# Performance work log

Measured on AMD Instinct MI355X. Metric: run time of the kernel, lower is better.

The kernel has to match this reference:

```python
import jax, jax.numpy as jnp
import numpy as np

NUM_HEADS = 16
ROPE_THETA = 10000.0


def _rope_angles(seq_len, head_dim, dtype):
    # lucidrains rotary_embedding_torch: freqs = theta^(-2i/d) for i in 0..d/2,
    # angles = pos * freq, then each angle repeated twice along last dim (interleaved pairs).
    inv_freq = 1.0 / (ROPE_THETA ** (jnp.arange(0, head_dim, 2, dtype=jnp.float32) / head_dim))
    angles = jnp.arange(seq_len, dtype=jnp.float32)[:, None] * inv_freq  # [N, D/2]
    return jnp.repeat(angles, 2, axis=-1).astype(dtype)  # [N, D]


def _rotate_half(t):
    # interleaved pairs: (x0, x1) -> (-x1, x0)
    t1 = t[..., ::2]
    t2 = t[..., 1::2]
    return jnp.stack([-t2, t1], axis=-1).reshape(t.shape)


def _apply_rope(t, cos, sin):
    # t: [B, H, N, D]; cos/sin: [N, D]
    return t * cos + _rotate_half(t) * sin


def setup_inputs() -> dict:
    key = jax.random.key(0)
    ks = jax.random.split(key, 5)
    B, N, C = 4, 1024, 1024
    return {
        "x": jax.random.normal(ks[0], (B, N, C), dtype=jnp.float32),
        "w_qkv": jax.random.normal(ks[1], (C, 3 * C), dtype=jnp.float32) * (C ** -0.5),
        "b_qkv": jax.random.normal(ks[2], (3 * C,), dtype=jnp.float32) * 0.02,
        "w_proj": jax.random.normal(ks[3], (C, C), dtype=jnp.float32) * (C ** -0.5),
        "b_proj": jax.random.normal(ks[4], (C,), dtype=jnp.float32) * 0.02,
    }


def reference(x, w_qkv, b_qkv, w_proj, b_proj):
    B, N, C = x.shape
    H = NUM_HEADS
    D = C // H

    qkv = x @ w_qkv + b_qkv  # [B, N, 3C]
    qkv = qkv.reshape(B, N, 3, H, D).transpose(2, 0, 3, 1, 4)  # [3, B, H, N, D]
    q, k, v = qkv[0], qkv[1], qkv[2]

    ang = _rope_angles(N, D, x.dtype)
    cos, sin = jnp.cos(ang), jnp.sin(ang)
    q = _apply_rope(q, cos, sin)
    k = _apply_rope(k, cos, sin)

    scale = D ** -0.5  # SDPA default scale
    scores = jnp.einsum("bhqd,bhkd->bhqk", q, k) * scale
    attn = jax.nn.softmax(scores, axis=-1)
    out = jnp.einsum("bhqk,bhkd->bhqd", attn, v)  # [B, H, N, D]

    out = out.transpose(0, 2, 1, 3).reshape(B, N, C)
    return out @ w_proj + b_proj
```

## Files before the change

kernel.cpp:

```cpp
#include <hip/hip_runtime.h>
#include <math.h>

#define BB 4
#define NN 1024
#define CC 1024
#define HH 16
#define DD 64
#define N3 3072

typedef __attribute__((ext_vector_type(8))) short bf16x8;
typedef __attribute__((ext_vector_type(8))) _Float16 f16x8;
typedef __attribute__((ext_vector_type(4))) _Float16 f16x4;
typedef __attribute__((ext_vector_type(4))) float f32x4;
typedef __attribute__((ext_vector_type(4))) unsigned int u32x4;

struct ushort4_t { unsigned short x, y, z, w; };

static __device__ __forceinline__ unsigned short f2b(float f) {
    union { float f; unsigned int u; } v; v.f = f;
    unsigned int r = (v.u + 0x7fffu + ((v.u >> 16) & 1u)) >> 16;
    return (unsigned short)r;
}

static __device__ __forceinline__ void ldg_lds16(const void* g, void* l) {
    __builtin_amdgcn_global_load_lds(
        (const __attribute__((address_space(1))) unsigned int*)g,
        (__attribute__((address_space(3))) unsigned int*)l, 16, 0, 0);
}

__global__ __launch_bounds__(256) void prep(const float* __restrict__ x,
                                            const float* __restrict__ wq,
                                            const float* __restrict__ wp,
                                            _Float16* __restrict__ Xh,
                                            _Float16* __restrict__ Wqt,
                                            _Float16* __restrict__ Wpt,
                                            float* __restrict__ ct,
                                            float* __restrict__ st) {
    const int blk = blockIdx.x;
    const int t = threadIdx.x;
    if (blk < 4096) {
        int tid = blk * 256 + t;
        float4 v = ((const float4*)x)[tid];
        f16x4 o = {(_Float16)v.x, (_Float16)v.y, (_Float16)v.z, (_Float16)v.w};
        ((f16x4*)Xh)[tid] = o;
    } else if (blk < 5632) {
        int idx = blk - 4096;
        int n  = (idx % 12) * 256 + t;
        int k0 = (idx / 12) * 8;
        f16x8 o;
        #pragma unroll
        for (int kk = 0; kk < 8; kk++)
            o[kk] = (_Float16)wq[(size_t)(k0 + kk) * N3 + n];
        *(f16x8*)(Wqt + (size_t)n * 1024 + k0) = o;
    } else if (blk < 6144) {
        int idx = blk - 5632;
        int n  = (idx % 4) * 256 + t;
        int k0 = (idx / 4) * 8;
        f16x8 o;
        #pragma unroll
        for (int kk = 0; kk < 8; kk++)
            o[kk] = (_Float16)wp[(size_t)(k0 + kk) * 1024 + n];
        *(f16x8*)(Wpt + (size_t)n * 1024 + k0) = o;
    } else {
        int tid = (blk - 6144) * 256 + t;
        int n = tid >> 5, i = tid & 31;
        double ang = (double)n * exp2(-(double)i * (13.287712379549449 / 32.0));
        ct[tid] = (float)cos(ang);
        st[tid] = (float)sin(ang);
    }
}

static __device__ __forceinline__ void gemm_body_pipe(const char* gA, const char* gB,
                                                      int m0, int n0,
                                                      _Float16* As0, _Float16* As1,
                                                      _Float16* Bs0, _Float16* Bs1,
                                                      int tid, int ln, int qd,
                                                      int wm, int wn, f32x4 acc[4][4]) {
    const int lrow   = tid >> 3;
    const int lchunk = tid & 7;
    const int swz    = (lchunk ^ (lrow & 7)) * 8;

    u32x4 pa[4], pb[4];

    #pragma unroll
    for (int c = 0; c < 4; c++) {
        size_t ra = (size_t)(m0 + c * 32 + lrow) * 2048 + lchunk * 16;
        size_t rb = (size_t)(n0 + c * 32 + lrow) * 2048 + lchunk * 16;
        pa[c] = *(const u32x4*)(gA + ra);
        pb[c] = *(const u32x4*)(gB + rb);
    }
    #pragma unroll
    for (int c = 0; c < 4; c++) {
        *(u32x4*)&As0[(c * 32 + lrow) * 64 + swz] = pa[c];
        *(u32x4*)&Bs0[(c * 32 + lrow) * 64 + swz] = pb[c];
    }
    #pragma unroll
    for (int c = 0; c < 4; c++) {
        size_t ra = (size_t)(m0 + c * 32 + lrow) * 2048 + 128 + lchunk * 16;
        size_t rb = (size_t)(n0 + c * 32 + lrow) * 2048 + 128 + lchunk * 16;
        pa[c] = *(const u32x4*)(gA + ra);
        pb[c] = *(const u32x4*)(gB + rb);
    }
    __syncthreads();

    #pragma unroll
    for (int t = 0; t < 16; t++) {
        const _Float16* Ac = (t & 1) ? As1 : As0;
        const _Float16* Bc = (t & 1) ? Bs1 : Bs0;

        #pragma unroll
        for (int kc = 0; kc < 2; kc++) {
            f16x8 af[4], bf[4];
            #pragma unroll
            for (int i = 0; i < 4; i++)
                af[i] = *(const f16x8*)&Ac[(wm + i * 16 + ln) * 64 +
                                           (((kc * 4 + qd) ^ (ln & 7)) * 8)];
            #pragma unroll
            for (int j = 0; j < 4; j++)
                bf[j] = *(const f16x8*)&Bc[(wn + j * 16 + ln) * 64 +
                                           (((kc * 4 + qd) ^ (ln & 7)) * 8)];
            #pragma unroll
            for (int i = 0; i < 4; i++)
                #pragma unroll
                for (int j = 0; j < 4; j++)
                    acc[i][j] = __builtin_amdgcn_mfma_f32_16x16x32_f16(af[i], bf[j],
                                                                       acc[i][j], 0, 0, 0);
        }

        if (t < 15) {
            _Float16* An = (t & 1) ? As0 : As1;
            _Float16* Bn = (t & 1) ? Bs0 : Bs1;
            #pragma unroll
            for (int c = 0; c < 4; c++) {
                *(u32x4*)&An[(c * 32 + lrow) * 64 + swz] = pa[c];
                *(u32x4*)&Bn[(c * 32 + lrow) * 64 + swz] = pb[c];
            }
            if (t < 14) {
                size_t ko = (size_t)(t + 2) * 128;
                #pragma unroll
                for (int c = 0; c < 4; c++) {
                    size_t ra = (size_t)(m0 + c * 32 + lrow) * 2048 + ko + lchunk * 16;
                    size_t rb = (size_t)(n0 + c * 32 + lrow) * 2048 + ko + lchunk * 16;
                    pa[c] = *(const u32x4*)(gA + ra);
                    pb[c] = *(const u32x4*)(gB + rb);
                }
            }
        }
        __syncthreads();
    }
}

static __device__ __forceinline__ void gemm_body_pipe_n64(const char* gA, const char* gB,
                                                          int m0, int n0,
                                                          _Float16* As0, _Float16* As1,
                                                          _Float16* Bs0, _Float16* Bs1,
                                                          int tid, int ln, int qd,
                                                          int wm, int wn, f32x4 acc[4][2]) {
    const int lrow   = tid >> 3;
    const int lchunk = tid & 7;
    const int swz    = (lchunk ^ (lrow & 7)) * 8;

    u32x4 pa[4], pb[2];

    #pragma unroll
    for (int c = 0; c < 4; c++)
        pa[c] = *(const u32x4*)(gA + (size_t)(m0 + c * 32 + lrow) * 2048 + lchunk * 16);
    #pragma unroll
    for (int c = 0; c < 2; c++)
        pb[c] = *(const u32x4*)(gB + (size_t)(n0 + c * 32 + lrow) * 2048 + lchunk * 16);
    #pragma unroll
    for (int c = 0; c < 4; c++)
        *(u32x4*)&As0[(c * 32 + lrow) * 64 + swz] = pa[c];
    #pragma unroll
    for (int c = 0; c < 2; c++)
        *(u32x4*)&Bs0[(c * 32 + lrow) * 64 + swz] = pb[c];
    #pragma unroll
    for (int c = 0; c < 4; c++)
        pa[c] = *(const u32x4*)(gA + (size_t)(m0 + c * 32 + lrow) * 2048 + 128 + lchunk * 16);
    #pragma unroll
    for (int c = 0; c < 2; c++)
        pb[c] = *(const u32x4*)(gB + (size_t)(n0 + c * 32 + lrow) * 2048 + 128 + lchunk * 16);
    __syncthreads();

    #pragma unroll
    for (int t = 0; t < 16; t++) {
        const _Float16* Ac = (t & 1) ? As1 : As0;
        const _Float16* Bc = (t & 1) ? Bs1 : Bs0;

        #pragma unroll
        for (int kc = 0; kc < 2; kc++) {
            f16x8 af[4], bf[2];
            #pragma unroll
            for (int i = 0; i < 4; i++)
                af[i] = *(const f16x8*)&Ac[(wm + i * 16 + ln) * 64 +
                                           (((kc * 4 + qd) ^ (ln & 7)) * 8)];
            #pragma unroll
            for (int j = 0; j < 2; j++)
                bf[j] = *(const f16x8*)&Bc[(wn + j * 16 + ln) * 64 +
                                           (((kc * 4 + qd) ^ (ln & 7)) * 8)];
            #pragma unroll
            for (int i = 0; i < 4; i++)
                #pragma unroll
                for (int j = 0; j < 2; j++)
                    acc[i][j] = __builtin_amdgcn_mfma_f32_16x16x32_f16(af[i], bf[j],
                                                                       acc[i][j], 0, 0, 0);
        }

        if (t < 15) {
            _Float16* An = (t & 1) ? As0 : As1;
            _Float16* Bn = (t & 1) ? Bs0 : Bs1;
            #pragma unroll
            for (int c = 0; c < 4; c++)
                *(u32x4*)&An[(c * 32 + lrow) * 64 + swz] = pa[c];
            #pragma unroll
            for (int c = 0; c < 2; c++)
                *(u32x4*)&Bn[(c * 32 + lrow) * 64 + swz] = pb[c];
            if (t < 14) {
                size_t ko = (size_t)(t + 2) * 128;
                #pragma unroll
                for (int c = 0; c < 4; c++)
                    pa[c] = *(const u32x4*)(gA + (size_t)(m0 + c * 32 + lrow) * 2048 + ko + lchunk * 16);
                #pragma unroll
                for (int c = 0; c < 2; c++)
                    pb[c] = *(const u32x4*)(gB + (size_t)(n0 + c * 32 + lrow) * 2048 + ko + lchunk * 16);
            }
        }
        __syncthreads();
    }
}

__global__ __launch_bounds__(256) void qkv_mfma(const _Float16* __restrict__ Ah,
                                                const _Float16* __restrict__ Bt,
                                                const float* __restrict__ bias,
                                                const float* __restrict__ cost,
                                                const float* __restrict__ sint,
                                                unsigned short* __restrict__ Q,
                                                unsigned short* __restrict__ K,
                                                unsigned short* __restrict__ Vtg) {
    __shared__ __align__(16) _Float16 As[2][128 * 64];
    __shared__ __align__(16) _Float16 Bs[2][128 * 64];
    const int t = threadIdx.x;
    const int lane = t & 63;
    const int w = t >> 6;
    const int ln = lane & 15, qd = lane >> 4;
    const int n0 = blockIdx.x * 128;
    const int m0 = blockIdx.y * 128;
    const int wm = (w >> 1) * 64, wn = (w & 1) * 64;

    f32x4 acc[4][4];
    #pragma unroll
    for (int i = 0; i < 4; i++)
        #pragma unroll
        for (int j = 0; j < 4; j++) acc[i][j] = (f32x4){0.f, 0.f, 0.f, 0.f};

    gemm_body_pipe((const char*)Ah, (const char*)Bt, m0, n0,
                   As[0], As[1], Bs[0], Bs[1], t, ln, qd, wm, wn, acc);

    const int s = n0 >> 10;
    const int h = ((n0 + wn) >> 6) & 15;
    if (s < 2) {
        unsigned short* dst = (s == 0) ? Q : K;
        const float sc0 = (s == 0) ? 0.125f : 1.0f;
        #pragma unroll
        for (int i = 0; i < 4; i++) {
            #pragma unroll
            for (int reg = 0; reg < 4; reg++) {
                int row = m0 + wm + i * 16 + qd * 4 + reg;
                int b = row >> 10, n = row & 1023;
                size_t obase = (((size_t)(b * HH + h)) * NN + n) * DD;
                #pragma unroll
                for (int j = 0; j < 4; j++) {
                    int d = j * 16 + ln;
                    float v = acc[i][j][reg] + bias[n0 + wn + d];
                    float pv = __shfl_xor(v, 1);
                    float cs = cost[n * 32 + (d >> 1)];
                    float sn = sint[n * 32 + (d >> 1)];
                    float outv = ((d & 1) ? (v * cs + pv * sn) : (v * cs - pv * sn)) * sc0;
                    dst[obase + d] = f2b(outv);
                }
            }
        }
    } else {
        #pragma unroll
        for (int i = 0; i < 4; i++) {
            int row0 = m0 + wm + i * 16 + qd * 4;
            int b = row0 >> 10, n = row0 & 1023;
            size_t tbase = ((size_t)(b * HH + h)) * DD * NN + n;
            #pragma unroll
            for (int j = 0; j < 4; j++) {
                int d = j * 16 + ln;
                float bb = bias[n0 + wn + d];
                ushort4_t pk;
                pk.x = f2b(acc[i][j][0] + bb);
                pk.y = f2b(acc[i][j][1] + bb);
                pk.z = f2b(acc[i][j][2] + bb);
                pk.w = f2b(acc[i][j][3] + bb);
                *(ushort4_t*)&Vtg[tbase + (size_t)d * NN] = pk;
            }
        }
    }
}

__global__ __launch_bounds__(256) void attn_flash(const unsigned short* __restrict__ Qb,
                                                  const unsigned short* __restrict__ Kb,
                                                  const unsigned short* __restrict__ Vtg,
                                                  _Float16* __restrict__ AO) {
    __shared__ __align__(16) unsigned short Ks[3][64 * 64];
    __shared__ __align__(16) unsigned short Vt[2][64 * 64];
    __shared__ __align__(16) unsigned short Ps[4][32 * 64];

    const int t    = threadIdx.x;
    const int lane = t & 63;
    const int w    = t >> 6;
    const int ln   = lane & 15;
    const int qd   = lane >> 4;
    const int bq   = blockIdx.x;
    const int h    = blockIdx.y;
    const int b    = blockIdx.z;
    const size_t base = (size_t)(b * HH + h) * NN * DD;
    const char* Kc = (const char*)(Kb + base);
    const char* Vc = (const char*)(Vtg + base);
    const int xorc = ((lane & 7) ^ (lane >> 3)) * 16;
    const int r8   = lane >> 3;
    const int wrow = w * 16;

    bf16x8 qf[2][2];
    #pragma unroll
    for (int g = 0; g < 2; g++) {
        const unsigned short* qp = Qb + base +
            (size_t)(bq * 128 + w * 32 + g * 16 + ln) * DD + qd * 8;
        qf[g][0] = *(const bf16x8*)qp;
        qf[g][1] = *(const bf16x8*)(qp + 32);
    }

    f32x4 o[2][5];
    #pragma unroll
    for (int g = 0; g < 2; g++)
        #pragma unroll
        for (int x = 0; x < 5; x++) o[g][x] = (f32x4){0.f, 0.f, 0.f, 0.f};

    bf16x8 onesf;
    #pragma unroll
    for (int x = 0; x < 8; x++) onesf[x] = (short)0x3F80;

    #pragma unroll
    for (int tile = 0; tile < 3; tile++)
        #pragma unroll
        for (int c = 0; c < 2; c++) {
            int rr = wrow + c * 8 + r8;
            ldg_lds16(Kc + (size_t)(tile * 64 + rr) * 128 + xorc,
                      &Ks[tile][(wrow + c * 8) * 64]);
        }
    #pragma unroll
    for (int tile = 0; tile < 2; tile++)
        #pragma unroll
        for (int c = 0; c < 2; c++) {
            int rr = wrow + c * 8 + r8;
            ldg_lds16(Vc + (size_t)rr * 2048 + (size_t)tile * 128 + xorc,
                      &Vt[tile][(wrow + c * 8) * 64]);
        }
    __syncthreads();

    f32x4 scur[2][4];
    {
        const unsigned short* KsB = Ks[0];
        #pragma unroll
        for (int j = 0; j < 4; j++) {
            bf16x8 k0f = *(const bf16x8*)&KsB[(ln + 16 * j) * 64 + ((qd ^ (ln & 7)) * 8)];
            bf16x8 k1f = *(const bf16x8*)&KsB[(ln + 16 * j) * 64 + (((4 + qd) ^ (ln & 7)) * 8)];
            #pragma unroll
            for (int g = 0; g < 2; g++) {
                f32x4 sj = {0.f, 0.f, 0.f, 0.f};
                sj = __builtin_amdgcn_mfma_f32_16x16x32_bf16(qf[g][0], k0f, sj, 0, 0, 0);
                sj = __builtin_amdgcn_mfma_f32_16x16x32_bf16(qf[g][1], k1f, sj, 0, 0, 0);
                scur[g][j] = sj;
            }
        }
    }

    const float C1 = 1.44269504f;
    const float C0 = -16.0f * 1.44269504f;

    #pragma unroll
    for (int tt = 0; tt < 16; tt++) {
        f32x4 snext[2][4];
        if (tt < 15) {
            const unsigned short* KsB = Ks[(tt + 1) % 3];
            #pragma unroll
            for (int j = 0; j < 4; j++) {
                bf16x8 k0f = *(const bf16x8*)&KsB[(ln + 16 * j) * 64 + ((qd ^ (ln & 7)) * 8)];
                bf16x8 k1f = *(const bf16x8*)&KsB[(ln + 16 * j) * 64 + (((4 + qd) ^ (ln & 7)) * 8)];
                #pragma unroll
                for (int g = 0; g < 2; g++) {
                    f32x4 sj = {0.f, 0.f, 0.f, 0.f};
                    sj = __builtin_amdgcn_mfma_f32_16x16x32_bf16(qf[g][0], k0f, sj, 0, 0, 0);
                    sj = __builtin_amdgcn_mfma_f32_16x16x32_bf16(qf[g][1], k1f, sj, 0, 0, 0);
                    snext[g][j] = sj;
                }
            }
        }

        unsigned short* PsB = &Ps[w][0];
        #pragma unroll
        for (int g = 0; g < 2; g++)
            #pragma unroll
            for (int j = 0; j < 4; j++)
                #pragma unroll
                for (int r = 0; r < 4; r++) {
                    float p = exp2f(fmaf(scur[g][j][r], C1, C0));
                    union { float f; unsigned int u; } cv; cv.f = p;
                    int m = g * 16 + qd * 4 + r;
                    PsB[m * 64 + ((((ln >> 3) + 2 * j) ^ (m & 7)) * 8) + (ln & 7)] =
                        (unsigned short)((cv.u + 0x8000u) >> 16);
                }

        {
            const unsigned short* VtB = Vt[tt & 1];
            bf16x8 pf[2][2];
            #pragma unroll
            for (int g = 0; g < 2; g++) {
                pf[g][0] = *(const bf16x8*)&PsB[(g * 16 + ln) * 64 + ((qd ^ (ln & 7)) * 8)];
                pf[g][1] = *(const bf16x8*)&PsB[(g * 16 + ln) * 64 + (((4 + qd) ^ (ln & 7)) * 8)];
            }
            #pragma unroll
            for (int j = 0; j < 4; j++) {
                bf16x8 v0f = *(const bf16x8*)&VtB[(ln + 16 * j) * 64 + ((qd ^ (ln & 7)) * 8)];
                bf16x8 v1f = *(const bf16x8*)&VtB[(ln + 16 * j) * 64 + (((4 + qd) ^ (ln & 7)) * 8)];
                #pragma unroll
                for (int g = 0; g < 2; g++) {
                    o[g][j] = __builtin_amdgcn_mfma_f32_16x16x32_bf16(pf[g][0], v0f, o[g][j], 0, 0, 0);
                    o[g][j] = __builtin_amdgcn_mfma_f32_16x16x32_bf16(pf[g][1], v1f, o[g][j], 0, 0, 0);
                }
            }
            #pragma unroll
            for (int g = 0; g < 2; g++) {
                o[g][4] = __builtin_amdgcn_mfma_f32_16x16x32_bf16(pf[g][0], onesf, o[g][4], 0, 0, 0);
                o[g][4] = __builtin_amdgcn_mfma_f32_16x16x32_bf16(pf[g][1], onesf, o[g][4], 0, 0, 0);
            }
        }

        __syncthreads();

        if (tt <= 12) {
            int tile = tt + 3;
            #pragma unroll
            for (int c = 0; c < 2; c++) {
                int rr = wrow + c * 8 + r8;
                ldg_lds16(Kc + (size_t)(tile * 64 + rr) * 128 + xorc,
                          &Ks[tt % 3][(wrow + c * 8) * 64]);
            }
        }
        if (tt <= 13) {
            int tile = tt + 2;
            #pragma unroll
            for (int c = 0; c < 2; c++) {
                int rr = wrow + c * 8 + r8;
                ldg_lds16(Vc + (size_t)rr * 2048 + (size_t)tile * 128 + xorc,
                          &Vt[tt & 1][(wrow + c * 8) * 64]);
            }
        }

        #pragma unroll
        for (int g = 0; g < 2; g++)
            #pragma unroll
            for (int j = 0; j < 4; j++) scur[g][j] = snext[g][j];
    }

    #pragma unroll
    for (int g = 0; g < 2; g++)
        #pragma unroll
        for (int r = 0; r < 4; r++) {
            float inv = 1.0f / o[g][4][r];
            int q = bq * 128 + w * 32 + g * 16 + qd * 4 + r;
            _Float16* op = AO + (((size_t)b * NN + q) * HH + h) * DD + ln;
            op[0]  = (_Float16)(o[g][0][r] * inv);
            op[16] = (_Float16)(o[g][1][r] * inv);
            op[32] = (_Float16)(o[g][2][r] * inv);
            op[48] = (_Float16)(o[g][3][r] * inv);
        }
}

__global__ __launch_bounds__(256) void proj_mfma(const _Float16* __restrict__ Ah,
                                                 const _Float16* __restrict__ Bt,
                                                 const float* __restrict__ bias,
                                                 float* __restrict__ out) {
    __shared__ __align__(16) _Float16 As[2][128 * 64];
    __shared__ __align__(16) _Float16 Bs[2][64 * 64];
    const int t = threadIdx.x;
    const int lane = t & 63;
    const int w = t >> 6;
    const int ln = lane & 15, qd = lane >> 4;
    const int n0 = blockIdx.x * 64;
    const int m0 = blockIdx.y * 128;
    const int wm = (w >> 1) * 64, wn = (w & 1) * 32;

    f32x4 acc[4][2];
    #pragma unroll
    for (int i = 0; i < 4; i++)
        #pragma unroll
        for (int j = 0; j < 2; j++) acc[i][j] = (f32x4){0.f, 0.f, 0.f, 0.f};

    gemm_body_pipe_n64((const char*)Ah, (const char*)Bt, m0, n0,
                       As[0], As[1], Bs[0], Bs[1], t, ln, qd, wm, wn, acc);

    #pragma unroll
    for (int i = 0; i < 4; i++) {
        #pragma unroll
        for (int reg = 0; reg < 4; reg++) {
            int row = m0 + wm + i * 16 + qd * 4 + reg;
            #pragma unroll
            for (int j = 0; j < 2; j++) {
                int col = n0 + wn + j * 16 + ln;
                out[(size_t)row * 1024 + col] = acc[i][j][reg] + bias[col];
            }
        }
    }
}

extern "C" void kernel_launch(void* const* d_in, const int* in_sizes, int n_in,
                              void* d_out, int out_size, void* d_ws, size_t ws_size,
                              hipStream_t stream) {
    const float* x      = (const float*)d_in[0];
    const float* w_qkv  = (const float*)d_in[1];
    const float* b_qkv  = (const float*)d_in[2];
    const float* w_proj = (const float*)d_in[3];
    const float* b_proj = (const float*)d_in[4];
    float* out = (float*)d_out;

    char* ws = (char*)d_ws;
    _Float16* Xh   = (_Float16*)(ws);
    _Float16* Wqt  = (_Float16*)(ws + (8u << 20));
    _Float16* Wpt  = (_Float16*)(ws + (14u << 20));
    unsigned short* Q  = (unsigned short*)(ws + (16u << 20));
    unsigned short* K  = (unsigned short*)(ws + (24u << 20));
    unsigned short* Vt = (unsigned short*)(ws + (32u << 20));
    _Float16* AOh  = (_Float16*)(ws + (40u << 20));
    float* cost    = (float*)(ws + (48u << 20));
    float* sint    = (float*)(ws + (48u << 20) + (128u << 10));

    prep<<<6272, 256, 0, stream>>>(x, w_qkv, w_proj, Xh, Wqt, Wpt, cost, sint);
    qkv_mfma<<<dim3(24, 32), 256, 0, stream>>>(Xh, Wqt, b_qkv, cost, sint, Q, K, Vt);
    attn_flash<<<dim3(8, 16, 4), 256, 0, stream>>>(Q, K, Vt, AOh);
    proj_mfma<<<dim3(16, 32), 256, 0, stream>>>(AOh, Wpt, b_proj, out);
}
```

Measured before the change: 182.3 us.

## Split attention over two key halves and merge partial results in a new kernel

The attention kernel now splits the key sequence into two halves across blocks, doubling the grid from 512 to 1024 blocks so more CUs are busy. Each half writes unnormalized fp32 partial outputs and row sums, and a new merge kernel adds them and normalizes into the fp16 buffer. Alongside this, the P tile in shared memory is shrunk to 16 rows per wave and reused per query group. The change adds a kernel launch and about 32 MB of fp32 partial-output traffic. The merge is valid because the kernel uses a fixed softmax offset rather than a running max.

New measurement: 186.6 us. 1.02x slower.

```diff
diff --git a/kernel.cpp b/kernel.cpp
--- a/kernel.cpp
+++ b/kernel.cpp
@@ -304,17 +304,19 @@
 __global__ __launch_bounds__(256) void attn_flash(const unsigned short* __restrict__ Qb,
                                                   const unsigned short* __restrict__ Kb,
                                                   const unsigned short* __restrict__ Vtg,
-                                                  _Float16* __restrict__ AO) {
+                                                  float* __restrict__ Op,
+                                                  float* __restrict__ lp) {
     __shared__ __align__(16) unsigned short Ks[3][64 * 64];
     __shared__ __align__(16) unsigned short Vt[2][64 * 64];
-    __shared__ __align__(16) unsigned short Ps[4][32 * 64];
+    __shared__ __align__(16) unsigned short Ps[4][16 * 64];
 
     const int t    = threadIdx.x;
     const int lane = t & 63;
     const int w    = t >> 6;
     const int ln   = lane & 15;
     const int qd   = lane >> 4;
-    const int bq   = blockIdx.x;
+    const int qt   = blockIdx.x >> 1;
+    const int kq   = blockIdx.x & 1;
     const int h    = blockIdx.y;
     const int b    = blockIdx.z;
     const size_t base = (size_t)(b * HH + h) * NN * DD;
@@ -323,12 +325,13 @@
     const int xorc = ((lane & 7) ^ (lane >> 3)) * 16;
     const int r8   = lane >> 3;
     const int wrow = w * 16;
+    const int kbase = kq * 512;
 
     bf16x8 qf[2][2];
     #pragma unroll
     for (int g = 0; g < 2; g++) {
         const unsigned short* qp = Qb + base +
-            (size_t)(bq * 128 + w * 32 + g * 16 + ln) * DD + qd * 8;
+            (size_t)(qt * 128 + w * 32 + g * 16 + ln) * DD + qd * 8;
         qf[g][0] = *(const bf16x8*)qp;
         qf[g][1] = *(const bf16x8*)(qp + 32);
     }
@@ -348,7 +351,7 @@
         #pragma unroll
         for (int c = 0; c < 2; c++) {
             int rr = wrow + c * 8 + r8;
-            ldg_lds16(Kc + (size_t)(tile * 64 + rr) * 128 + xorc,
+            ldg_lds16(Kc + (size_t)(kbase + tile * 64 + rr) * 128 + xorc,
                       &Ks[tile][(wrow + c * 8) * 64]);
         }
     #pragma unroll
@@ -356,7 +359,7 @@
         #pragma unroll
         for (int c = 0; c < 2; c++) {
             int rr = wrow + c * 8 + r8;
-            ldg_lds16(Vc + (size_t)rr * 2048 + (size_t)tile * 128 + xorc,
+            ldg_lds16(Vc + (size_t)rr * 2048 + (size_t)(kbase + tile * 64) * 2 + xorc,
                       &Vt[tile][(wrow + c * 8) * 64]);
         }
     __syncthreads();
@@ -382,9 +385,9 @@
     const float C0 = -16.0f * 1.44269504f;
 
     #pragma unroll
-    for (int tt = 0; tt < 16; tt++) {
+    for (int tt = 0; tt < 8; tt++) {
         f32x4 snext[2][4];
-        if (tt < 15) {
+        if (tt < 7) {
             const unsigned short* KsB = Ks[(tt + 1) % 3];
             #pragma unroll
             for (int j = 0; j < 4; j++) {
@@ -400,62 +403,56 @@
             }
         }
 
-        unsigned short* PsB = &Ps[w][0];
-        #pragma unroll
-        for (int g = 0; g < 2; g++)
-            #pragma unroll
-            for (int j = 0; j < 4; j++)
-                #pragma unroll
-                for (int r = 0; r < 4; r++) {
-                    float p = exp2f(fmaf(scur[g][j][r], C1, C0));
-                    union { float f; unsigned int u; } cv; cv.f = p;
-                    int m = g * 16 + qd * 4 + r;
-                    PsB[m * 64 + ((((ln >> 3) + 2 * j) ^ (m & 7)) * 8) + (ln & 7)] =
-                        (unsigned short)((cv.u + 0x8000u) >> 16);
-                }
-
         {
             const unsigned short* VtB = Vt[tt & 1];
-            bf16x8 pf[2][2];
+            bf16x8 v0f[4], v1f[4];
+            #pragma unroll
+            for (int j = 0; j < 4; j++) {
+                v0f[j] = *(const bf16x8*)&VtB[(ln + 16 * j) * 64 + ((qd ^ (ln & 7)) * 8)];
+                v1f[j] = *(const bf16x8*)&VtB[(ln + 16 * j) * 64 + (((4 + qd) ^ (ln & 7)) * 8)];
+            }
+            unsigned short* PsB = &Ps[w][0];
             #pragma unroll
             for (int g = 0; g < 2; g++) {
-                pf[g][0] = *(const bf16x8*)&PsB[(g * 16 + ln) * 64 + ((qd ^ (ln & 7)) * 8)];
-                pf[g][1] = *(const bf16x8*)&PsB[(g * 16 + ln) * 64 + (((4 + qd) ^ (ln & 7)) * 8)];
-            }
-            #pragma unroll
-            for (int j = 0; j < 4; j++) {
-                bf16x8 v0f = *(const bf16x8*)&VtB[(ln + 16 * j) * 64 + ((qd ^ (ln & 7)) * 8)];
-                bf16x8 v1f = *(const bf16x8*)&VtB[(ln + 16 * j) * 64 + (((4 + qd) ^ (ln & 7)) * 8)];
-                #pragma unroll
-                for (int g = 0; g < 2; g++) {
-                    o[g][j] = __builtin_amdgcn_mfma_f32_16x16x32_bf16(pf[g][0], v0f, o[g][j], 0, 0, 0);
-                    o[g][j] = __builtin_amdgcn_mfma_f32_16x16x32_bf16(pf[g][1], v1f, o[g][j], 0, 0, 0);
+                #pragma unroll
+                for (int j = 0; j < 4; j++)
+                    #pragma unroll
+                    for (int r = 0; r < 4; r++) {
+                        float p = exp2f(fmaf(scur[g][j][r], C1, C0));
+                        union { float f; unsigned int u; } cv; cv.f = p;
+                        int m = qd * 4 + r;
+                        PsB[m * 64 + ((((ln >> 3) + 2 * j) ^ (m & 7)) * 8) + (ln & 7)] =
+                            (unsigned short)((cv.u + 0x8000u) >> 16);
+                    }
+                bf16x8 pf0 = *(const bf16x8*)&PsB[ln * 64 + ((qd ^ (ln & 7)) * 8)];
+                bf16x8 pf1 = *(const bf16x8*)&PsB[ln * 64 + (((4 + qd) ^ (ln & 7)) * 8)];
+                #pragma unroll
+                for (int j = 0; j < 4; j++) {
+                    o[g][j] = __builtin_amdgcn_mfma_f32_16x16x32_bf16(pf0, v0f[j], o[g][j], 0, 0, 0);
+                    o[g][j] = __builtin_amdgcn_mfma_f32_16x16x32_bf16(pf1, v1f[j], o[g][j], 0, 0, 0);
                 }
-            }
-            #pragma unroll
-            for (int g = 0; g < 2; g++) {
-                o[g][4] = __builtin_amdgcn_mfma_f32_16x16x32_bf16(pf[g][0], onesf, o[g][4], 0, 0, 0);
-                o[g][4] = __builtin_amdgcn_mfma_f32_16x16x32_bf16(pf[g][1], onesf, o[g][4], 0, 0, 0);
+                o[g][4] = __builtin_amdgcn_mfma_f32_16x16x32_bf16(pf0, onesf, o[g][4], 0, 0, 0);
+                o[g][4] = __builtin_amdgcn_mfma_f32_16x16x32_bf16(pf1, onesf, o[g][4], 0, 0, 0);
             }
         }
 
         __syncthreads();
 
-        if (tt <= 12) {
+        if (tt <= 4) {
             int tile = tt + 3;
             #pragma unroll
             for (int c = 0; c < 2; c++) {
                 int rr = wrow + c * 8 + r8;
-                ldg_lds16(Kc + (size_t)(tile * 64 + rr) * 128 + xorc,
+                ldg_lds16(Kc + (size_t)(kbase + tile * 64 + rr) * 128 + xorc,
                           &Ks[tt % 3][(wrow + c * 8) * 64]);
             }
         }
-        if (tt <= 13) {
+        if (tt <= 5) {
             int tile = tt + 2;
             #pragma unroll
             for (int c = 0; c < 2; c++) {
                 int rr = wrow + c * 8 + r8;
-                ldg_lds16(Vc + (size_t)rr * 2048 + (size_t)tile * 128 + xorc,
+                ldg_lds16(Vc + (size_t)rr * 2048 + (size_t)(kbase + tile * 64) * 2 + xorc,
                           &Vt[tt & 1][(wrow + c * 8) * 64]);
             }
         }
@@ -470,14 +467,31 @@
     for (int g = 0; g < 2; g++)
         #pragma unroll
         for (int r = 0; r < 4; r++) {
-            float inv = 1.0f / o[g][4][r];
-            int q = bq * 128 + w * 32 + g * 16 + qd * 4 + r;
-            _Float16* op = AO + (((size_t)b * NN + q) * HH + h) * DD + ln;
-            op[0]  = (_Float16)(o[g][0][r] * inv);
-            op[16] = (_Float16)(o[g][1][r] * inv);
-            op[32] = (_Float16)(o[g][2][r] * inv);
-            op[48] = (_Float16)(o[g][3][r] * inv);
-        }
+            int q = qt * 128 + w * 32 + g * 16 + qd * 4 + r;
+            size_t rb = (((size_t)b * NN + q) * HH + h) * DD;
+            float* op = Op + (size_t)kq * 4194304 + rb + ln;
+            op[0]  = o[g][0][r];
+            op[16] = o[g][1][r];
+            op[32] = o[g][2][r];
+            op[48] = o[g][3][r];
+            if (ln == 0)
+                lp[kq * 65536 + (((size_t)b * NN + q) * HH + h)] = o[g][4][r];
+        }
+}
+
+__global__ __launch_bounds__(256) void merge_kernel(const float* __restrict__ O1,
+                                                    const float* __restrict__ O2,
+                                                    const float* __restrict__ l1,
+                                                    const float* __restrict__ l2,
+                                                    _Float16* __restrict__ AO) {
+    int i = blockIdx.x * 256 + threadIdx.x;
+    float4 a = ((const float4*)O1)[i];
+    float4 c = ((const float4*)O2)[i];
+    int row = i >> 4;
+    float inv = 1.0f / (l1[row] + l2[row]);
+    f16x4 o = {(_Float16)((a.x + c.x) * inv), (_Float16)((a.y + c.y) * inv),
+               (_Float16)((a.z + c.z) * inv), (_Float16)((a.w + c.w) * inv)};
+    ((f16x4*)AO)[i] = o;
 }
 
 __global__ __launch_bounds__(256) void proj_mfma(const _Float16* __restrict__ Ah,
@@ -537,9 +551,12 @@
     _Float16* AOh  = (_Float16*)(ws + (40u << 20));
     float* cost    = (float*)(ws + (48u << 20));
     float* sint    = (float*)(ws + (48u << 20) + (128u << 10));
+    float* Opf     = (float*)(ws + (56u << 20));
+    float* lpf     = (float*)(ws + (88u << 20));
 
     prep<<<6272, 256, 0, stream>>>(x, w_qkv, w_proj, Xh, Wqt, Wpt, cost, sint);
     qkv_mfma<<<dim3(24, 32), 256, 0, stream>>>(Xh, Wqt, b_qkv, cost, sint, Q, K, Vt);
-    attn_flash<<<dim3(8, 16, 4), 256, 0, stream>>>(Q, K, Vt, AOh);
+    attn_flash<<<dim3(16, 16, 4), 256, 0, stream>>>(Q, K, Vt, Opf, lpf);
+    merge_kernel<<<4096, 256, 0, stream>>>(Opf, Opf + 4194304, lpf, lpf + 65536, AOh);
     proj_mfma<<<dim3(16, 32), 256, 0, stream>>>(AOh, Wpt, b_proj, out);
 }
```
